# Kernel optimization log

Measured on AMD Instinct MI355X. Metric: run time of the kernel, lower is better.

Reference implementation:

```python
import jax, jax.numpy as jnp
import numpy as np

B, W, H, V, L = 64, 512, 1024, 32000, 2


def setup_inputs() -> dict:
    key = jax.random.key(0)
    ks = jax.random.split(key, 20)
    s = 0.02  # init scale
    n = lambda k, shp: jax.random.normal(k, shp, jnp.float32)
    return {
        "input": jax.random.randint(ks[0], (B, 1), 0, V),
        "h0": n(ks[1], (L, B, H)),
        "c0": n(ks[2], (L, B, H)),
        "encoder_output": n(ks[3], (B, W, H)),
        "embedding": n(ks[4], (V, H)) * s,
        "W_ih0": n(ks[5], (4 * H, H)) * s,
        "W_hh0": n(ks[6], (4 * H, H)) * s,
        "b_ih0": n(ks[7], (4 * H,)) * s,
        "b_hh0": n(ks[8], (4 * H,)) * s,
        "W_ih1": n(ks[9], (4 * H, H)) * s,
        "W_hh1": n(ks[10], (4 * H, H)) * s,
        "b_ih1": n(ks[11], (4 * H,)) * s,
        "b_hh1": n(ks[12], (4 * H,)) * s,
        "att_w": n(ks[13], (2 * H,)) * s,
        "att_b": n(ks[14], (1,)) * s,
        "input_W": n(ks[15], (H, 2 * H)) * s,
        "input_b": n(ks[16], (H,)) * s,
        "out_W": n(ks[17], (V, H)) * s,
        "out_b": n(ks[18], (V,)) * s,
    }


def _lstm_step(x, h, c, W_ih, W_hh, b_ih, b_hh):
    # PyTorch gate order: i, f, g, o
    g = x @ W_ih.T + h @ W_hh.T + b_ih + b_hh
    i, f, gg, o = jnp.split(g, 4, axis=-1)
    c2 = jax.nn.sigmoid(f) * c + jax.nn.sigmoid(i) * jnp.tanh(gg)
    return jax.nn.sigmoid(o) * jnp.tanh(c2), c2


def reference(input, h0, c0, encoder_output, embedding,
              W_ih0, W_hh0, b_ih0, b_hh0, W_ih1, W_hh1, b_ih1, b_hh1,
              att_w, att_b, input_W, input_b, out_W, out_b):
    Hd = h0.shape[-1]
    emb = embedding[input]                       # (B,1,H)
    att_state = h0[-1] * c0[-1]                  # (B,H)
    # Vectorized replacement of the per-word cat+linear loop:
    # att_line(cat(enc_w, att_state)) = enc_w @ w_enc + att_state @ w_st + b
    w_enc, w_st = att_w[:Hd], att_w[Hd:]
    scores = encoder_output @ w_enc + (att_state @ w_st)[:, None] + att_b[0]  # (B,W)
    # Original quirk: weigth starts with a zeros column, then softmax over
    # weigth[:, 0:-1] -> zero column + scores for words 0..W-2 (last dropped).
    zeros = jnp.zeros((scores.shape[0], 1), scores.dtype)
    full = jnp.concatenate([zeros, scores[:, :-1]], axis=1)  # (B,W)
    wts = jax.nn.softmax(full, axis=1)
    ctx = jnp.einsum('bw,bwh->bh', wts, encoder_output)      # (B,H)
    x = jnp.concatenate([ctx, emb[:, 0, :]], axis=-1)        # (B,2H)
    x = x @ input_W.T + input_b                              # (B,H)
    h1, c1 = _lstm_step(x, h0[0], c0[0], W_ih0, W_hh0, b_ih0, b_hh0)
    h2, c2 = _lstm_step(h1, h0[1], c0[1], W_ih1, W_hh1, b_ih1, b_hh1)
    logits = h2 @ out_W.T + out_b                            # (B,V)
    logp = jax.nn.log_softmax(logits, axis=-1)[:, None, :]   # (B,1,V)
    return logp, jnp.stack([h1, h2]), jnp.stack([c1, c2])
```

## Files before the change

kernel.cpp:

```cpp
#include <hip/hip_runtime.h>
#include <hip/hip_bf16.h>

#define Bsz 64
#define Wln 512
#define Hd  1024
#define Vc  32000

typedef short v8s __attribute__((ext_vector_type(8)));
typedef float f32x4 __attribute__((ext_vector_type(4)));

__device__ inline unsigned short f2b(float f) {
  union { float f; unsigned u; } v; v.f = f;
  return (unsigned short)((v.u + 0x8000u) >> 16);
}
__device__ inline float wave_sum(float v) {
  #pragma unroll
  for (int o = 32; o; o >>= 1) v += __shfl_down(v, o);
  return v;
}
__device__ inline float wave_max(float v) {
  #pragma unroll
  for (int o = 32; o; o >>= 1) v = fmaxf(v, __shfl_down(v, o));
  return v;
}
__device__ inline float wave_sum_all(float v) {
  #pragma unroll
  for (int o = 32; o; o >>= 1) v += __shfl_xor(v, o);
  return v;
}
__device__ inline float wave_max_all(float v) {
  #pragma unroll
  for (int o = 32; o; o >>= 1) v = fmaxf(v, __shfl_xor(v, o));
  return v;
}
__device__ inline float sigm(float x) { return 1.f / (1.f + expf(-x)); }

__device__ inline v8s cvt_frag(float4 x0, float4 x1) {
  v8s r;
  r[0] = (short)f2b(x0.x); r[1] = (short)f2b(x0.y);
  r[2] = (short)f2b(x0.z); r[3] = (short)f2b(x0.w);
  r[4] = (short)f2b(x1.x); r[5] = (short)f2b(x1.y);
  r[6] = (short)f2b(x1.z); r[7] = (short)f2b(x1.w);
  return r;
}

__device__ inline void stage_A(const float* __restrict__ A, const float* __restrict__ Ab,
                               int sA, char* pool, int tid) {
  #pragma unroll
  for (int it = 0; it < 16; ++it) {
    int idx = it * 512 + tid;
    int row = idx >> 7, ch = idx & 127;
    const float* src = A + (size_t)row * sA + ch * 8;
    float4 x0 = *(const float4*)src;
    float4 x1 = *(const float4*)(src + 4);
    if (Ab) {
      const float* s2 = Ab + (size_t)row * sA + ch * 8;
      float4 y0 = *(const float4*)s2;
      float4 y1 = *(const float4*)(s2 + 4);
      x0.x += y0.x; x0.y += y0.y; x0.z += y0.z; x0.w += y0.w;
      x1.x += y1.x; x1.y += y1.y; x1.z += y1.z; x1.w += y1.w;
    }
    *(v8s*)(pool + row * 2048 + ((ch * 16) ^ ((row & 7) << 4))) = cvt_frag(x0, x1);
  }
}

__global__ __launch_bounds__(512, 4) void k_attn(
    const float* __restrict__ enc, const float* __restrict__ att_w,
    const float* __restrict__ h0, const float* __restrict__ c0,
    const float* __restrict__ att_b,
    float* __restrict__ ctxp, float* __restrict__ pm_a, float* __restrict__ ps_a)
{
  __shared__ __align__(16) float pool[17 * 1024];
  __shared__ float fullv[16];
  __shared__ float redA[8];
  const int b = blockIdx.x >> 5, ch = blockIdx.x & 31;
  const int c0r = ch * 16;
  const int tid = threadIdx.x, w = tid >> 6, lane = tid & 63;
  const float* encb = enc + (size_t)b * Wln * Hd;

  #pragma unroll
  for (int it = 0; it < 9; ++it) {
    int idx = it * 512 + tid;
    if (idx < 4352) {
      int rl = idx >> 8, c4 = idx & 255;
      int gr = c0r - 1 + rl;
      gr = gr < 0 ? 0 : gr;
      float4 v = *(const float4*)(encb + (size_t)gr * Hd + c4 * 4);
      *(float4*)(pool + rl * 1024 + c4 * 4) = v;
    }
  }

  {
    size_t base = (size_t)(Bsz + b) * Hd;
    int j = tid * 2;
    float s = h0[base + j] * c0[base + j] * att_w[Hd + j]
            + h0[base + j + 1] * c0[base + j + 1] * att_w[Hd + j + 1];
    s = wave_sum(s);
    if (lane == 0) redA[w] = s;
  }
  __syncthreads();
  float sa = att_b[0];
  #pragma unroll
  for (int i = 0; i < 8; ++i) sa += redA[i];

  float4 aw[4];
  #pragma unroll
  for (int s4 = 0; s4 < 4; ++s4)
    aw[s4] = *(const float4*)(att_w + s4 * 256 + lane * 4);

  #pragma unroll
  for (int k = 0; k < 2; ++k) {
    int lj = w * 2 + k;
    int j = c0r + lj;
    float v = 0.f;
    if (j > 0) {
      const float* rp = pool + lj * 1024;
      float s = 0.f;
      #pragma unroll
      for (int s4 = 0; s4 < 4; ++s4) {
        float4 e = *(const float4*)(rp + s4 * 256 + lane * 4);
        s += e.x * aw[s4].x + e.y * aw[s4].y + e.z * aw[s4].z + e.w * aw[s4].w;
      }
      s = wave_sum(s);
      v = s + sa;
    }
    if (lane == 0) fullv[lj] = v;
  }
  __syncthreads();

  float mv = (lane < 16) ? fullv[lane] : -1e30f;
  float M = wave_max_all(mv);
  float ev = (lane < 16) ? expf(mv - M) : 0.f;
  float S = wave_sum_all(ev);

  float4 a4[4] = {{0,0,0,0},{0,0,0,0},{0,0,0,0},{0,0,0,0}};
  #pragma unroll
  for (int k = 0; k < 2; ++k) {
    float wt = expf(fullv[w * 2 + k] - M);
    const float* rp = pool + (w * 2 + k + 1) * 1024;
    #pragma unroll
    for (int s4 = 0; s4 < 4; ++s4) {
      float4 e = *(const float4*)(rp + s4 * 256 + lane * 4);
      a4[s4].x += wt * e.x; a4[s4].y += wt * e.y;
      a4[s4].z += wt * e.z; a4[s4].w += wt * e.w;
    }
  }
  __syncthreads();
  #pragma unroll
  for (int s4 = 0; s4 < 4; ++s4)
    *(float4*)(pool + w * 1024 + s4 * 256 + lane * 4) = a4[s4];
  __syncthreads();

  for (int c = tid; c < Hd; c += 512) {
    float s = 0.f;
    #pragma unroll
    for (int ww = 0; ww < 8; ++ww) s += pool[ww * 1024 + c];
    ctxp[(size_t)(b * 32 + ch) * Hd + c] = s;
  }
  if (tid == 0) { pm_a[b * 32 + ch] = M; ps_a[b * 32 + ch] = S; }
}

__global__ __launch_bounds__(512) void k_ctx_fin(
    const float* __restrict__ ctxp, const float* __restrict__ pm_a,
    const float* __restrict__ ps_a, const int* __restrict__ input,
    const float* __restrict__ emb, float* __restrict__ cat)
{
  int b = blockIdx.x, tid = threadIdx.x;
  float Mg = pm_a[b * 32];
  #pragma unroll
  for (int c = 1; c < 32; ++c) Mg = fmaxf(Mg, pm_a[b * 32 + c]);
  float Sg = 0.f;
  float sc[32];
  #pragma unroll
  for (int c = 0; c < 32; ++c) {
    sc[c] = expf(pm_a[b * 32 + c] - Mg);
    Sg += ps_a[b * 32 + c] * sc[c];
  }
  float inv = 1.f / Sg;
  for (int h = tid; h < Hd; h += 512) {
    float s = 0.f;
    #pragma unroll
    for (int c = 0; c < 32; ++c) s += ctxp[(size_t)(b * 32 + c) * Hd + h] * sc[c];
    cat[b * 2 * Hd + h] = s * inv;
  }
  int idx = input[b];
  for (int j = tid; j < Hd; j += 512)
    cat[b * 2 * Hd + Hd + j] = emb[(size_t)idx * Hd + j];
}

__global__ __launch_bounds__(512) void k_input_gemm(
    const float* __restrict__ cat, const float* __restrict__ inW,
    const float* __restrict__ inb, float* __restrict__ x1, float* __restrict__ x2)
{
  __shared__ __align__(16) char pool[131072];
  const int tid = threadIdx.x;
  const int w = tid >> 6, lane = tid & 63;
  const int r = lane & 15, q = lane >> 4;
  const int kh = w;
  const int half = (blockIdx.x >= 64);
  const int n0 = (blockIdx.x & 63) * 16;
  const float* A = cat + half * 1024;
  const float* B = inW + half * 1024;
  float* out = half ? x2 : x1;

  const float* bp = B + (size_t)(n0 + r) * 2048 + kh * 128 + q * 8;
  float4 breg[4][2];
  #pragma unroll
  for (int kk = 0; kk < 4; ++kk) {
    breg[kk][0] = *(const float4*)(bp + kk * 32);
    breg[kk][1] = *(const float4*)(bp + kk * 32 + 4);
  }
  stage_A(A, nullptr, 2048, pool, tid);
  __syncthreads();

  f32x4 acc[4] = {{0,0,0,0},{0,0,0,0},{0,0,0,0},{0,0,0,0}};
  const int swz = (r & 7) << 4;
  #pragma unroll
  for (int kk = 0; kk < 4; ++kk) {
    v8s bf = cvt_frag(breg[kk][0], breg[kk][1]);
    int cb = ((kh * 128 + kk * 32 + q * 8) * 2) ^ swz;
    #pragma unroll
    for (int m = 0; m < 4; ++m) {
      v8s af = *(const v8s*)(pool + (m * 16 + r) * 2048 + cb);
      acc[m] = __builtin_amdgcn_mfma_f32_16x16x32_bf16(af, bf, acc[m], 0, 0, 0);
    }
  }
  __syncthreads();

  float (*red)[64][17] = (float(*)[64][17])pool;
  #pragma unroll
  for (int m = 0; m < 4; ++m)
    #pragma unroll
    for (int rr = 0; rr < 4; ++rr)
      red[w][lane][m * 4 + rr] = acc[m][rr];
  __syncthreads();

  #pragma unroll
  for (int it = 0; it < 2; ++it) {
    int e = it * 512 + tid;
    int cc = e & 15, rowi = e >> 4;
    int idx = ((rowi >> 4) << 2) + (rowi & 3);
    int le  = (((rowi >> 2) & 3) << 4) + cc;
    float s = 0.f;
    #pragma unroll
    for (int j = 0; j < 8; ++j) s += red[j][le][idx];
    float bb = half ? 0.f : inb[n0 + cc];
    out[(size_t)rowi * Hd + n0 + cc] = s + bb;
  }
}

__global__ __launch_bounds__(512) void k_gate_lstm(
    const float* __restrict__ xA, const float* __restrict__ xAb,
    const float* __restrict__ hA,
    const float* __restrict__ W_ih, const float* __restrict__ W_hh,
    const float* __restrict__ b_ih, const float* __restrict__ b_hh,
    const float* __restrict__ c0,
    float* __restrict__ out_h, float* __restrict__ out_c)
{
  __shared__ __align__(16) char pool[131072];
  const int tid = threadIdx.x;
  const int w = tid >> 6, lane = tid & 63;
  const int r = lane & 15, q = lane >> 4;
  const int kh = w;
  const int gate = r >> 2, jl = r & 3;
  const size_t Brow = (size_t)gate * Hd + blockIdx.x * 4 + jl;

  float4 breg[2][4][2];
  {
    const float* bp0 = W_ih + Brow * Hd + kh * 128 + q * 8;
    const float* bp1 = W_hh + Brow * Hd + kh * 128 + q * 8;
    #pragma unroll
    for (int kk = 0; kk < 4; ++kk) {
      breg[0][kk][0] = *(const float4*)(bp0 + kk * 32);
      breg[0][kk][1] = *(const float4*)(bp0 + kk * 32 + 4);
      breg[1][kk][0] = *(const float4*)(bp1 + kk * 32);
      breg[1][kk][1] = *(const float4*)(bp1 + kk * 32 + 4);
    }
  }

  f32x4 acc[4] = {{0,0,0,0},{0,0,0,0},{0,0,0,0},{0,0,0,0}};
  const float* Amat[2] = { xA, hA };
  const float* Abm[2]  = { xAb, nullptr };
  #pragma unroll
  for (int p = 0; p < 2; ++p) {
    stage_A(Amat[p], Abm[p], Hd, pool, tid);
    __syncthreads();
    const int swz = (r & 7) << 4;
    #pragma unroll
    for (int kk = 0; kk < 4; ++kk) {
      v8s bf = cvt_frag(breg[p][kk][0], breg[p][kk][1]);
      int cb = ((kh * 128 + kk * 32 + q * 8) * 2) ^ swz;
      #pragma unroll
      for (int m = 0; m < 4; ++m) {
        v8s af = *(const v8s*)(pool + (m * 16 + r) * 2048 + cb);
        acc[m] = __builtin_amdgcn_mfma_f32_16x16x32_bf16(af, bf, acc[m], 0, 0, 0);
      }
    }
    __syncthreads();
  }

  float (*red)[64][17] = (float(*)[64][17])pool;
  #pragma unroll
  for (int m = 0; m < 4; ++m)
    #pragma unroll
    for (int rr = 0; rr < 4; ++rr)
      red[w][lane][m * 4 + rr] = acc[m][rr];
  __syncthreads();

  if (tid < 256) {
    int b = tid >> 2, jl2 = tid & 3;
    int jg = blockIdx.x * 4 + jl2;
    float gv[4];
    #pragma unroll
    for (int g2 = 0; g2 < 4; ++g2) {
      int cc = g2 * 4 + jl2;
      int idx = ((b >> 4) << 2) + (b & 3);
      int le  = (((b >> 2) & 3) << 4) + cc;
      float s = 0.f;
      #pragma unroll
      for (int j = 0; j < 8; ++j) s += red[j][le][idx];
      gv[g2] = s + b_ih[(size_t)g2 * Hd + jg] + b_hh[(size_t)g2 * Hd + jg];
    }
    float c = sigm(gv[1]) * c0[(size_t)b * Hd + jg] + sigm(gv[0]) * tanhf(gv[2]);
    float h = sigm(gv[3]) * tanhf(c);
    out_h[(size_t)b * Hd + jg] = h;
    out_c[(size_t)b * Hd + jg] = c;
  }
}

__global__ __launch_bounds__(512) void k_logits(
    const float* __restrict__ A, const float* __restrict__ B,
    const float* __restrict__ bias, float* __restrict__ out,
    float* __restrict__ pm, float* __restrict__ ps)
{
  __shared__ __align__(16) char pool[131072];
  const int tid = threadIdx.x;
  const int w = tid >> 6, lane = tid & 63;
  const int r = lane & 15, q = lane >> 4;
  const int nsub = w & 3, kh = w >> 2;
  const int n0 = blockIdx.x * 64;

  const float* bp = B + (size_t)(n0 + nsub * 16 + r) * Hd + kh * 512 + q * 8;
  float4 breg[16][2];
  #pragma unroll
  for (int kk = 0; kk < 16; ++kk) {
    breg[kk][0] = *(const float4*)(bp + kk * 32);
    breg[kk][1] = *(const float4*)(bp + kk * 32 + 4);
  }
  stage_A(A, nullptr, Hd, pool, tid);
  __syncthreads();

  f32x4 acc[4] = {{0,0,0,0},{0,0,0,0},{0,0,0,0},{0,0,0,0}};
  const int swz = (r & 7) << 4;
  #pragma unroll
  for (int kk = 0; kk < 16; ++kk) {
    v8s bf = cvt_frag(breg[kk][0], breg[kk][1]);
    int cb = ((kh * 512 + kk * 32 + q * 8) * 2) ^ swz;
    #pragma unroll
    for (int m = 0; m < 4; ++m) {
      v8s af = *(const v8s*)(pool + (m * 16 + r) * 2048 + cb);
      acc[m] = __builtin_amdgcn_mfma_f32_16x16x32_bf16(af, bf, acc[m], 0, 0, 0);
    }
  }
  __syncthreads();

  float (*red)[64][17] = (float(*)[64][17])pool;
  #pragma unroll
  for (int m = 0; m < 4; ++m)
    #pragma unroll
    for (int rr = 0; rr < 4; ++rr)
      red[w][lane][m * 4 + rr] = acc[m][rr];
  __syncthreads();

  #pragma unroll
  for (int it = 0; it < 8; ++it) {
    int e = it * 512 + tid;
    int cc = e & 63, rowi = e >> 6;
    int ns2 = cc >> 4, lo = cc & 15;
    int idx = ((rowi >> 4) << 2) + (rowi & 3);
    int le  = (((rowi >> 2) & 3) << 4) + lo;
    float val = red[ns2][le][idx] + red[ns2 + 4][le][idx] + bias[n0 + cc];
    out[(size_t)rowi * Vc + n0 + cc] = val;
    float wm = wave_max_all(val);
    float we = wave_sum_all(expf(val - wm));
    if (cc == 0) { pm[blockIdx.x * 64 + rowi] = wm; ps[blockIdx.x * 64 + rowi] = we; }
  }
}

__global__ __launch_bounds__(512) void k_lsm_sub(
    float* __restrict__ lg, const float* __restrict__ pm, const float* __restrict__ ps)
{
  __shared__ float redA[8], redB[8];
  int b = blockIdx.x >> 2, qc = blockIdx.x & 3;
  int tid = threadIdx.x, w = tid >> 6, lane = tid & 63;
  float m = -1e30f;
  for (int j = tid; j < 500; j += 512) m = fmaxf(m, pm[j * 64 + b]);
  m = wave_max(m);
  if (lane == 0) redA[w] = m;
  __syncthreads();
  float M = redA[0];
  #pragma unroll
  for (int i = 1; i < 8; ++i) M = fmaxf(M, redA[i]);
  float s = 0.f;
  for (int j = tid; j < 500; j += 512) s += ps[j * 64 + b] * expf(pm[j * 64 + b] - M);
  s = wave_sum(s);
  if (lane == 0) redB[w] = s;
  __syncthreads();
  float S = redB[0];
  #pragma unroll
  for (int i = 1; i < 8; ++i) S += redB[i];
  float lse = M + logf(S);
  float* row = lg + (size_t)b * Vc + qc * 8000;
  for (int j = tid * 4; j < 8000; j += 2048) {
    float4 v = *(const float4*)(row + j);
    v.x -= lse; v.y -= lse; v.z -= lse; v.w -= lse;
    *(float4*)(row + j) = v;
  }
}

extern "C" void kernel_launch(void* const* d_in, const int* in_sizes, int n_in,
                              void* d_out, int out_size, void* d_ws, size_t ws_size,
                              hipStream_t stream)
{
  const int*   input = (const int*)d_in[0];
  const float* h0    = (const float*)d_in[1];
  const float* c0    = (const float*)d_in[2];
  const float* enc   = (const float*)d_in[3];
  const float* emb   = (const float*)d_in[4];
  const float* W_ih0 = (const float*)d_in[5];
  const float* W_hh0 = (const float*)d_in[6];
  const float* b_ih0 = (const float*)d_in[7];
  const float* b_hh0 = (const float*)d_in[8];
  const float* W_ih1 = (const float*)d_in[9];
  const float* W_hh1 = (const float*)d_in[10];
  const float* b_ih1 = (const float*)d_in[11];
  const float* b_hh1 = (const float*)d_in[12];
  const float* att_w = (const float*)d_in[13];
  const float* att_b = (const float*)d_in[14];
  const float* inW   = (const float*)d_in[15];
  const float* inb   = (const float*)d_in[16];
  const float* outW  = (const float*)d_in[17];
  const float* outb  = (const float*)d_in[18];
  float* out = (float*)d_out;

  char* ws = (char*)d_ws;
  float* cat    = (float*)(ws + 0);
  float* x1     = (float*)(ws + 524288);
  float* x2     = (float*)(ws + 786432);
  float* ctxp   = (float*)(ws + 1048576);
  float* pm_a   = (float*)(ws + 9437184);
  float* ps_a   = (float*)(ws + 9445376);
  float* pm     = (float*)(ws + 9453568);
  float* ps     = (float*)(ws + 9584640);

  float* out_h = out + (size_t)Bsz * Vc;
  float* out_c = out_h + 2 * Bsz * Hd;
  float* h1 = out_h;
  float* h2 = out_h + Bsz * Hd;

  k_attn<<<Bsz * 32, 512, 0, stream>>>(enc, att_w, h0, c0, att_b, ctxp, pm_a, ps_a);
  k_ctx_fin<<<Bsz, 512, 0, stream>>>(ctxp, pm_a, ps_a, input, emb, cat);
  k_input_gemm<<<128, 512, 0, stream>>>(cat, inW, inb, x1, x2);
  k_gate_lstm<<<256, 512, 0, stream>>>(x1, x2, h0, W_ih0, W_hh0, b_ih0, b_hh0,
                                       c0, h1, out_c);
  k_gate_lstm<<<256, 512, 0, stream>>>(h1, nullptr, h0 + (size_t)Bsz * Hd,
                                       W_ih1, W_hh1, b_ih1, b_hh1,
                                       c0 + (size_t)Bsz * Hd, h2, out_c + Bsz * Hd);
  k_logits<<<500, 512, 0, stream>>>(h2, outW, outb, out, pm, ps);
  k_lsm_sub<<<256, 512, 0, stream>>>(out, pm, ps);
}
```

Baseline: 143.0 us.

## Pre-convert activations to bf16 in global memory and drop LDS staging in GEMMs

Producer kernels (ctx finalize, input GEMM, LSTM gates) now write bf16 copies of their activations, and every downstream GEMM reads its MFMA A-fragments straight from global memory instead of staging and converting fp32 tiles in 128KB of shared memory. This removes the per-block fp32 load and convert of the whole activation matrix, and the small LDS footprint lets several blocks share a CU. The input GEMM now covers the full K=2048 in one block, which removes the separate x1/x2 split. The logits kernel uses 32-column tiles over 1000 blocks for more parallelism, with half-wave softmax partials. The cost is uncoalesced global A reads that depend on cache hits, plus bf16 rounding of intermediate activations.

```diff
diff --git a/kernel.cpp b/kernel.cpp
--- a/kernel.cpp
+++ b/kernel.cpp
@@ -31,6 +31,16 @@
 __device__ inline float wave_max_all(float v) {
   #pragma unroll
   for (int o = 32; o; o >>= 1) v = fmaxf(v, __shfl_xor(v, o));
+  return v;
+}
+__device__ inline float half_sum(float v) {
+  #pragma unroll
+  for (int o = 16; o; o >>= 1) v += __shfl_xor(v, o);
+  return v;
+}
+__device__ inline float half_max(float v) {
+  #pragma unroll
+  for (int o = 16; o; o >>= 1) v = fmaxf(v, __shfl_xor(v, o));
   return v;
 }
 __device__ inline float sigm(float x) { return 1.f / (1.f + expf(-x)); }
@@ -42,26 +52,6 @@
   r[4] = (short)f2b(x1.x); r[5] = (short)f2b(x1.y);
   r[6] = (short)f2b(x1.z); r[7] = (short)f2b(x1.w);
   return r;
-}
-
-__device__ inline void stage_A(const float* __restrict__ A, const float* __restrict__ Ab,
-                               int sA, char* pool, int tid) {
-  #pragma unroll
-  for (int it = 0; it < 16; ++it) {
-    int idx = it * 512 + tid;
-    int row = idx >> 7, ch = idx & 127;
-    const float* src = A + (size_t)row * sA + ch * 8;
-    float4 x0 = *(const float4*)src;
-    float4 x1 = *(const float4*)(src + 4);
-    if (Ab) {
-      const float* s2 = Ab + (size_t)row * sA + ch * 8;
-      float4 y0 = *(const float4*)s2;
-      float4 y1 = *(const float4*)(s2 + 4);
-      x0.x += y0.x; x0.y += y0.y; x0.z += y0.z; x0.w += y0.w;
-      x1.x += y1.x; x1.y += y1.y; x1.z += y1.z; x1.w += y1.w;
-    }
-    *(v8s*)(pool + row * 2048 + ((ch * 16) ^ ((row & 7) << 4))) = cvt_frag(x0, x1);
-  }
 }
 
 __global__ __launch_bounds__(512, 4) void k_attn(
@@ -163,7 +153,8 @@
 __global__ __launch_bounds__(512) void k_ctx_fin(
     const float* __restrict__ ctxp, const float* __restrict__ pm_a,
     const float* __restrict__ ps_a, const int* __restrict__ input,
-    const float* __restrict__ emb, float* __restrict__ cat)
+    const float* __restrict__ emb, const float* __restrict__ h0,
+    ushort* __restrict__ catb, ushort* __restrict__ h0b)
 {
   int b = blockIdx.x, tid = threadIdx.x;
   float Mg = pm_a[b * 32];
@@ -181,53 +172,46 @@
     float s = 0.f;
     #pragma unroll
     for (int c = 0; c < 32; ++c) s += ctxp[(size_t)(b * 32 + c) * Hd + h] * sc[c];
-    cat[b * 2 * Hd + h] = s * inv;
+    catb[b * 2 * Hd + h] = f2b(s * inv);
   }
   int idx = input[b];
-  for (int j = tid; j < Hd; j += 512)
-    cat[b * 2 * Hd + Hd + j] = emb[(size_t)idx * Hd + j];
-}
-
-__global__ __launch_bounds__(512) void k_input_gemm(
-    const float* __restrict__ cat, const float* __restrict__ inW,
-    const float* __restrict__ inb, float* __restrict__ x1, float* __restrict__ x2)
-{
-  __shared__ __align__(16) char pool[131072];
+  for (int j = tid; j < Hd; j += 512) {
+    catb[b * 2 * Hd + Hd + j] = f2b(emb[(size_t)idx * Hd + j]);
+    h0b[b * Hd + j] = f2b(h0[(size_t)b * Hd + j]);
+    h0b[(Bsz + b) * Hd + j] = f2b(h0[(size_t)(Bsz + b) * Hd + j]);
+  }
+}
+
+__global__ __launch_bounds__(512, 4) void k_input_gemm(
+    const ushort* __restrict__ catb, const float* __restrict__ inW,
+    const float* __restrict__ inb, ushort* __restrict__ xb)
+{
+  __shared__ float red[8][64][17];
   const int tid = threadIdx.x;
   const int w = tid >> 6, lane = tid & 63;
   const int r = lane & 15, q = lane >> 4;
   const int kh = w;
-  const int half = (blockIdx.x >= 64);
-  const int n0 = (blockIdx.x & 63) * 16;
-  const float* A = cat + half * 1024;
-  const float* B = inW + half * 1024;
-  float* out = half ? x2 : x1;
-
-  const float* bp = B + (size_t)(n0 + r) * 2048 + kh * 128 + q * 8;
-  float4 breg[4][2];
-  #pragma unroll
-  for (int kk = 0; kk < 4; ++kk) {
+  const int n0 = blockIdx.x * 16;
+
+  const float* bp = inW + (size_t)(n0 + r) * 2048 + kh * 256 + q * 8;
+  float4 breg[8][2];
+  #pragma unroll
+  for (int kk = 0; kk < 8; ++kk) {
     breg[kk][0] = *(const float4*)(bp + kk * 32);
     breg[kk][1] = *(const float4*)(bp + kk * 32 + 4);
   }
-  stage_A(A, nullptr, 2048, pool, tid);
-  __syncthreads();
 
   f32x4 acc[4] = {{0,0,0,0},{0,0,0,0},{0,0,0,0},{0,0,0,0}};
-  const int swz = (r & 7) << 4;
-  #pragma unroll
-  for (int kk = 0; kk < 4; ++kk) {
+  #pragma unroll
+  for (int kk = 0; kk < 8; ++kk) {
     v8s bf = cvt_frag(breg[kk][0], breg[kk][1]);
-    int cb = ((kh * 128 + kk * 32 + q * 8) * 2) ^ swz;
     #pragma unroll
     for (int m = 0; m < 4; ++m) {
-      v8s af = *(const v8s*)(pool + (m * 16 + r) * 2048 + cb);
+      v8s af = *(const v8s*)(catb + (size_t)(m * 16 + r) * 2048 + kh * 256 + kk * 32 + q * 8);
       acc[m] = __builtin_amdgcn_mfma_f32_16x16x32_bf16(af, bf, acc[m], 0, 0, 0);
     }
   }
-  __syncthreads();
-
-  float (*red)[64][17] = (float(*)[64][17])pool;
+
   #pragma unroll
   for (int m = 0; m < 4; ++m)
     #pragma unroll
@@ -244,20 +228,18 @@
     float s = 0.f;
     #pragma unroll
     for (int j = 0; j < 8; ++j) s += red[j][le][idx];
-    float bb = half ? 0.f : inb[n0 + cc];
-    out[(size_t)rowi * Hd + n0 + cc] = s + bb;
-  }
-}
-
-__global__ __launch_bounds__(512) void k_gate_lstm(
-    const float* __restrict__ xA, const float* __restrict__ xAb,
-    const float* __restrict__ hA,
+    xb[(size_t)rowi * Hd + n0 + cc] = f2b(s + inb[n0 + cc]);
+  }
+}
+
+__global__ __launch_bounds__(512, 4) void k_gate_lstm(
+    const ushort* __restrict__ xA, const ushort* __restrict__ hA,
     const float* __restrict__ W_ih, const float* __restrict__ W_hh,
     const float* __restrict__ b_ih, const float* __restrict__ b_hh,
     const float* __restrict__ c0,
-    float* __restrict__ out_h, float* __restrict__ out_c)
-{
-  __shared__ __align__(16) char pool[131072];
+    float* __restrict__ out_h, float* __restrict__ out_c, ushort* __restrict__ houtb)
+{
+  __shared__ float red[8][64][17];
   const int tid = threadIdx.x;
   const int w = tid >> 6, lane = tid & 63;
   const int r = lane & 15, q = lane >> 4;
@@ -279,27 +261,20 @@
   }
 
   f32x4 acc[4] = {{0,0,0,0},{0,0,0,0},{0,0,0,0},{0,0,0,0}};
-  const float* Amat[2] = { xA, hA };
-  const float* Abm[2]  = { xAb, nullptr };
+  const ushort* Am[2] = { xA, hA };
   #pragma unroll
   for (int p = 0; p < 2; ++p) {
-    stage_A(Amat[p], Abm[p], Hd, pool, tid);
-    __syncthreads();
-    const int swz = (r & 7) << 4;
     #pragma unroll
     for (int kk = 0; kk < 4; ++kk) {
       v8s bf = cvt_frag(breg[p][kk][0], breg[p][kk][1]);
-      int cb = ((kh * 128 + kk * 32 + q * 8) * 2) ^ swz;
       #pragma unroll
       for (int m = 0; m < 4; ++m) {
-        v8s af = *(const v8s*)(pool + (m * 16 + r) * 2048 + cb);
+        v8s af = *(const v8s*)(Am[p] + (size_t)(m * 16 + r) * Hd + kh * 128 + kk * 32 + q * 8);
         acc[m] = __builtin_amdgcn_mfma_f32_16x16x32_bf16(af, bf, acc[m], 0, 0, 0);
       }
     }
-    __syncthreads();
-  }
-
-  float (*red)[64][17] = (float(*)[64][17])pool;
+  }
+
   #pragma unroll
   for (int m = 0; m < 4; ++m)
     #pragma unroll
@@ -325,46 +300,41 @@
     float h = sigm(gv[3]) * tanhf(c);
     out_h[(size_t)b * Hd + jg] = h;
     out_c[(size_t)b * Hd + jg] = c;
-  }
-}
-
-__global__ __launch_bounds__(512) void k_logits(
-    const float* __restrict__ A, const float* __restrict__ B,
+    houtb[(size_t)b * Hd + jg] = f2b(h);
+  }
+}
+
+__global__ __launch_bounds__(512, 4) void k_logits(
+    const ushort* __restrict__ A, const float* __restrict__ B,
     const float* __restrict__ bias, float* __restrict__ out,
     float* __restrict__ pm, float* __restrict__ ps)
 {
-  __shared__ __align__(16) char pool[131072];
+  __shared__ float red[8][64][17];
   const int tid = threadIdx.x;
   const int w = tid >> 6, lane = tid & 63;
   const int r = lane & 15, q = lane >> 4;
-  const int nsub = w & 3, kh = w >> 2;
-  const int n0 = blockIdx.x * 64;
-
-  const float* bp = B + (size_t)(n0 + nsub * 16 + r) * Hd + kh * 512 + q * 8;
-  float4 breg[16][2];
-  #pragma unroll
-  for (int kk = 0; kk < 16; ++kk) {
+  const int nsub = w & 1, kh = w >> 1;
+  const int n0 = blockIdx.x * 32;
+
+  const float* bp = B + (size_t)(n0 + nsub * 16 + r) * Hd + kh * 256 + q * 8;
+  float4 breg[8][2];
+  #pragma unroll
+  for (int kk = 0; kk < 8; ++kk) {
     breg[kk][0] = *(const float4*)(bp + kk * 32);
     breg[kk][1] = *(const float4*)(bp + kk * 32 + 4);
   }
-  stage_A(A, nullptr, Hd, pool, tid);
-  __syncthreads();
 
   f32x4 acc[4] = {{0,0,0,0},{0,0,0,0},{0,0,0,0},{0,0,0,0}};
-  const int swz = (r & 7) << 4;
-  #pragma unroll
-  for (int kk = 0; kk < 16; ++kk) {
+  #pragma unroll
+  for (int kk = 0; kk < 8; ++kk) {
     v8s bf = cvt_frag(breg[kk][0], breg[kk][1]);
-    int cb = ((kh * 512 + kk * 32 + q * 8) * 2) ^ swz;
     #pragma unroll
     for (int m = 0; m < 4; ++m) {
-      v8s af = *(const v8s*)(pool + (m * 16 + r) * 2048 + cb);
+      v8s af = *(const v8s*)(A + (size_t)(m * 16 + r) * Hd + kh * 256 + kk * 32 + q * 8);
       acc[m] = __builtin_amdgcn_mfma_f32_16x16x32_bf16(af, bf, acc[m], 0, 0, 0);
     }
   }
-  __syncthreads();
-
-  float (*red)[64][17] = (float(*)[64][17])pool;
+
   #pragma unroll
   for (int m = 0; m < 4; ++m)
     #pragma unroll
@@ -373,17 +343,20 @@
   __syncthreads();
 
   #pragma unroll
-  for (int it = 0; it < 8; ++it) {
+  for (int it = 0; it < 4; ++it) {
     int e = it * 512 + tid;
-    int cc = e & 63, rowi = e >> 6;
+    int cc = e & 31, rowi = e >> 5;
     int ns2 = cc >> 4, lo = cc & 15;
     int idx = ((rowi >> 4) << 2) + (rowi & 3);
     int le  = (((rowi >> 2) & 3) << 4) + lo;
-    float val = red[ns2][le][idx] + red[ns2 + 4][le][idx] + bias[n0 + cc];
+    float s = 0.f;
+    #pragma unroll
+    for (int j = 0; j < 4; ++j) s += red[ns2 + j * 2][le][idx];
+    float val = s + bias[n0 + cc];
     out[(size_t)rowi * Vc + n0 + cc] = val;
-    float wm = wave_max_all(val);
-    float we = wave_sum_all(expf(val - wm));
-    if (cc == 0) { pm[blockIdx.x * 64 + rowi] = wm; ps[blockIdx.x * 64 + rowi] = we; }
+    float hm = half_max(val);
+    float he = half_sum(expf(val - hm));
+    if ((lane & 31) == 0) { pm[blockIdx.x * 64 + rowi] = hm; ps[blockIdx.x * 64 + rowi] = he; }
   }
 }
 
@@ -394,7 +367,7 @@
   int b = blockIdx.x >> 2, qc = blockIdx.x & 3;
   int tid = threadIdx.x, w = tid >> 6, lane = tid & 63;
   float m = -1e30f;
-  for (int j = tid; j < 500; j += 512) m = fmaxf(m, pm[j * 64 + b]);
+  for (int j = tid; j < 1000; j += 512) m = fmaxf(m, pm[j * 64 + b]);
   m = wave_max(m);
   if (lane == 0) redA[w] = m;
   __syncthreads();
@@ -402,7 +375,7 @@
   #pragma unroll
   for (int i = 1; i < 8; ++i) M = fmaxf(M, redA[i]);
   float s = 0.f;
-  for (int j = tid; j < 500; j += 512) s += ps[j * 64 + b] * expf(pm[j * 64 + b] - M);
+  for (int j = tid; j < 1000; j += 512) s += ps[j * 64 + b] * expf(pm[j * 64 + b] - M);
   s = wave_sum(s);
   if (lane == 0) redB[w] = s;
   __syncthreads();
@@ -444,14 +417,16 @@
   float* out = (float*)d_out;
 
   char* ws = (char*)d_ws;
-  float* cat    = (float*)(ws + 0);
-  float* x1     = (float*)(ws + 524288);
-  float* x2     = (float*)(ws + 786432);
-  float* ctxp   = (float*)(ws + 1048576);
-  float* pm_a   = (float*)(ws + 9437184);
-  float* ps_a   = (float*)(ws + 9445376);
-  float* pm     = (float*)(ws + 9453568);
-  float* ps     = (float*)(ws + 9584640);
+  ushort* catb = (ushort*)(ws + 0);
+  ushort* xb   = (ushort*)(ws + 262144);
+  ushort* h0b  = (ushort*)(ws + 393216);
+  ushort* h1b  = (ushort*)(ws + 655360);
+  ushort* h2b  = (ushort*)(ws + 786432);
+  float* ctxp  = (float*)(ws + 1048576);
+  float* pm_a  = (float*)(ws + 9437184);
+  float* ps_a  = (float*)(ws + 9445376);
+  float* pm    = (float*)(ws + 9453568);
+  float* ps    = (float*)(ws + 9709568);
 
   float* out_h = out + (size_t)Bsz * Vc;
   float* out_c = out_h + 2 * Bsz * Hd;
@@ -459,13 +434,13 @@
   float* h2 = out_h + Bsz * Hd;
 
   k_attn<<<Bsz * 32, 512, 0, stream>>>(enc, att_w, h0, c0, att_b, ctxp, pm_a, ps_a);
-  k_ctx_fin<<<Bsz, 512, 0, stream>>>(ctxp, pm_a, ps_a, input, emb, cat);
-  k_input_gemm<<<128, 512, 0, stream>>>(cat, inW, inb, x1, x2);
-  k_gate_lstm<<<256, 512, 0, stream>>>(x1, x2, h0, W_ih0, W_hh0, b_ih0, b_hh0,
-                                       c0, h1, out_c);
-  k_gate_lstm<<<256, 512, 0, stream>>>(h1, nullptr, h0 + (size_t)Bsz * Hd,
-                                       W_ih1, W_hh1, b_ih1, b_hh1,
-                                       c0 + (size_t)Bsz * Hd, h2, out_c + Bsz * Hd);
-  k_logits<<<500, 512, 0, stream>>>(h2, outW, outb, out, pm, ps);
+  k_ctx_fin<<<Bsz, 512, 0, stream>>>(ctxp, pm_a, ps_a, input, emb, h0, catb, h0b);
+  k_input_gemm<<<64, 512, 0, stream>>>(catb, inW, inb, xb);
+  k_gate_lstm<<<256, 512, 0, stream>>>(xb, h0b, W_ih0, W_hh0, b_ih0, b_hh0,
+                                       c0, h1, out_c, h1b);
+  k_gate_lstm<<<256, 512, 0, stream>>>(h1b, h0b + Bsz * Hd, W_ih1, W_hh1,
+                                       b_ih1, b_hh1, c0 + (size_t)Bsz * Hd,
+                                       h2, out_c + Bsz * Hd, h2b);
+  k_logits<<<1000, 512, 0, stream>>>(h2b, outW, outb, out, pm, ps);
   k_lsm_sub<<<256, 512, 0, stream>>>(out, pm, ps);
 }
```

Measured after the change: 155.2 us. 8.5% more time.
